# Performance work log

Hardware: AMD Instinct MI355X
Metric: run time of the kernel (lower is better)

The kernel has to match this reference:

```python
import jax, jax.numpy as jnp
import numpy as np

T = 16384       # tokens (flattened leading dims)
D_IN = 1024     # in_features
D_OUT = 1024    # out_features
E = 8           # n_models (experts)


def setup_inputs() -> dict:
    key = jax.random.key(0)
    kx, ki, kw, kb = jax.random.split(key, 4)
    x = jax.random.normal(kx, (T, D_IN), dtype=jnp.float32)
    idxs = jax.random.randint(ki, (T,), 0, E, dtype=jnp.int32)
    # Per-expert Linear params (nn.Linear default-ish init scale)
    scale = 1.0 / np.sqrt(D_IN)
    W = jax.random.uniform(kw, (E, D_IN, D_OUT), dtype=jnp.float32, minval=-scale, maxval=scale)
    b = jax.random.uniform(kb, (E, D_OUT), dtype=jnp.float32, minval=-scale, maxval=scale)
    return {"x": x, "idxs": idxs, "W": W, "b": b}


def reference(x, idxs, W, b):
    # Original: for each expert i, y[idxs==i] = Linear_i(x[idxs==i]); return relu(y).
    # Equivalent math: each token t gets expert idxs[t]'s linear.
    # Compute all experts densely (E is small), then gather the assigned row.
    ys = jnp.einsum('ti,eio->eto', x, W) + b[:, None, :]   # [E, T, D_OUT]
    y = ys[idxs, jnp.arange(x.shape[0])]                    # [T, D_OUT] pick assigned expert
    return jax.nn.relu(y)
```

## Files before the change

kernel.cpp:

```cpp
#include <hip/hip_runtime.h>
#include <hip/hip_bf16.h>
#include <stdint.h>


#define T_TOK 16384
#define DIN   1024
#define DOUT  1024
#define NE    8
#define BM    128
#define BN    128
#define BK    64
#define TPX   17
#define MAX_TILES 136
#define MP_MAX (T_TOK + NE * BM)

typedef __attribute__((ext_vector_type(8))) short short8;
typedef __attribute__((ext_vector_type(4))) short short4v;
typedef __attribute__((ext_vector_type(4))) float floatx4;
typedef __attribute__((ext_vector_type(4))) int int4v;

__device__ __forceinline__ short f2b(float f) {
  return __builtin_bit_cast(short, __float2bfloat16(f));
}
__device__ __forceinline__ float b2f(unsigned short u) {
  unsigned v = ((unsigned)u) << 16;
  return __builtin_bit_cast(float, v);
}
__device__ __forceinline__ void glds16(const void* g, void* l) {
  __builtin_amdgcn_global_load_lds(
      (__attribute__((address_space(1))) void*)g,
      (__attribute__((address_space(3))) void*)l, 16, 0, 0);
}

#define FLAG_OFF    0
#define NTILES_OFF  64
#define TABLE_OFF   1024
#define TPAD_OFF    8192
#define WT_OFF      81920
#define XB_OFF      16859136
#define WS_NEED     (16859136UL + (size_t)T_TOK * DIN * 2)

#define TRANS_BLOCKS 512
#define CONV_BLOCKS  1024

__global__ __launch_bounds__(1024) void k_front(
    const unsigned short* __restrict__ xu, const int* __restrict__ idxs,
    const void* __restrict__ Wsrc, short* __restrict__ Wt, short* __restrict__ xb,
    int* __restrict__ flag, int* __restrict__ ntiles,
    int4v* __restrict__ table, int* __restrict__ tpad) {
  __shared__ int fS;
  __shared__ unsigned short tile[128][130];
  __shared__ int wtot[16][NE], waveBase[16][NE];
  __shared__ int totS[NE], padS[NE + 1];

  int tid = threadIdx.x;
  if (tid == 0) fS = 0;
  __syncthreads();
  if (tid < 256) {
    int ex = (xu[tid] >> 7) & 0xFF;
    if (ex >= 0xC0) atomicOr(&fS, 1);
  }
  __syncthreads();
  int fp32 = fS;

  if (blockIdx.x >= 1 + TRANS_BLOCKS) {
    if (!fp32) return;
    int b2 = blockIdx.x - (1 + TRANS_BLOCKS);
    size_t base = ((size_t)b2 * 1024 + tid) * 16;
    const float* src = (const float*)xu + base;
    floatx4 a0 = *(const floatx4*)(src + 0);
    floatx4 a1 = *(const floatx4*)(src + 4);
    floatx4 a2 = *(const floatx4*)(src + 8);
    floatx4 a3 = *(const floatx4*)(src + 12);
    short8 o0, o1;
    #pragma unroll
    for (int j = 0; j < 4; ++j) {
      o0[j] = f2b(a0[j]); o0[4 + j] = f2b(a1[j]);
      o1[j] = f2b(a2[j]); o1[4 + j] = f2b(a3[j]);
    }
    *(short8*)(xb + base) = o0;
    *(short8*)(xb + base + 8) = o1;
    return;
  }

  if (blockIdx.x != 0) {
    int b = blockIdx.x - 1;
    int e = b >> 6, kt = (b >> 3) & 7, nt8 = b & 7;
    size_t ibase = (size_t)e * DIN * DOUT + (size_t)(kt * 128) * DOUT + nt8 * 128;
    int k = tid >> 3, n16 = (tid & 7) * 16;
    if (fp32) {
      const float* p = (const float*)Wsrc + ibase + (size_t)k * DOUT + n16;
      #pragma unroll
      for (int g = 0; g < 4; ++g) {
        floatx4 a = *(const floatx4*)(p + g * 4);
        #pragma unroll
        for (int j = 0; j < 4; ++j) tile[k][n16 + g * 4 + j] = (unsigned short)f2b(a[j]);
      }
    } else {
      const short* p = (const short*)Wsrc + ibase + (size_t)k * DOUT + n16;
      #pragma unroll
      for (int g = 0; g < 2; ++g) {
        short8 v = *(const short8*)(p + g * 8);
        #pragma unroll
        for (int j = 0; j < 8; ++j) tile[k][n16 + g * 8 + j] = (unsigned short)v[j];
      }
    }
    __syncthreads();
    int n = tid >> 3, k16 = (tid & 7) * 16;
    short8 o0, o1;
    #pragma unroll
    for (int j = 0; j < 8; ++j) {
      o0[j] = (short)tile[k16 + j][n];
      o1[j] = (short)tile[k16 + 8 + j][n];
    }
    size_t obase = (size_t)e * DOUT * DIN + (size_t)(nt8 * 128 + n) * DIN + kt * 128 + k16;
    *(short8*)(Wt + obase) = o0;
    *(short8*)(Wt + obase + 8) = o1;
    return;
  }

  int lane = tid & 63, w = tid >> 6;
  if (tid == 0) *flag = fp32;

  int c[NE];
  #pragma unroll
  for (int e = 0; e < NE; ++e) c[e] = 0;
  const int4v* iv = (const int4v*)idxs;
  int4v vv[4];
  #pragma unroll
  for (int it = 0; it < 4; ++it) {
    vv[it] = iv[tid * 4 + it];
    ++c[vv[it].x]; ++c[vv[it].y]; ++c[vv[it].z]; ++c[vv[it].w];
  }
  int incl[NE];
  #pragma unroll
  for (int e = 0; e < NE; ++e) {
    incl[e] = c[e];
    #pragma unroll
    for (int d = 1; d < 64; d <<= 1) {
      int o = __shfl_up(incl[e], d);
      if (lane >= d) incl[e] += o;
    }
  }
  if (lane == 63) {
    #pragma unroll
    for (int e = 0; e < NE; ++e) wtot[w][e] = incl[e];
  }
  __syncthreads();
  if (tid < NE) {
    int s = 0;
    for (int ww = 0; ww < 16; ++ww) s += wtot[ww][tid];
    totS[tid] = s;
  }
  __syncthreads();
  if (tid == 0) {
    int p = 0, tc = 0;
    for (int e = 0; e < NE; ++e) {
      padS[e] = p;
      int cn = totS[e];
      int nmt = (cn + BM - 1) >> 7;
      for (int m = 0; m < nmt; ++m) table[tc++] = (int4v){e, p + m * BM, 0, 0};
      p += nmt * BM;
    }
    padS[NE] = p;
    *ntiles = tc;
  }
  __syncthreads();
  if (tid < 128) {
    int ww = tid >> 3, e = tid & 7;
    int s = padS[e];
    for (int wp = 0; wp < ww; ++wp) s += wtot[wp][e];
    waveBase[ww][e] = s;
  }
  __syncthreads();
  int base[NE];
  #pragma unroll
  for (int e = 0; e < NE; ++e) base[e] = waveBase[w][e] + incl[e] - c[e];
  #pragma unroll
  for (int it = 0; it < 4; ++it) {
    #pragma unroll
    for (int cm = 0; cm < 4; ++cm) {
      int te = vv[it][cm];
      int tk = tid * 16 + it * 4 + cm;
      #pragma unroll
      for (int e0 = 0; e0 < NE; ++e0)
        if (te == e0) tpad[base[e0]++] = tk;
    }
  }
  #pragma unroll
  for (int e = 0; e < NE; ++e) {
    int start = padS[e] + totS[e];
    int len = padS[e + 1] - start;
    if (tid < len) tpad[start + tid] = -1;
  }
}

__launch_bounds__(256, 4)
__global__ void k_gemm(const void* __restrict__ xv, const short* __restrict__ xb,
                       const void* __restrict__ bv,
                       const short* __restrict__ Wt, const int* __restrict__ tpad,
                       const int* __restrict__ ntilesp, const int4v* __restrict__ table,
                       const int* __restrict__ flagp, void* __restrict__ outv) {
  int bid = blockIdx.x;
  int xcd = bid & 7;
  int s = bid >> 3;
  int nt = s & 7;
  int ti = s >> 3;
  int t = xcd * TPX + ti;
  if (t >= *ntilesp) return;
  int4v te = table[t];
  int e = te.x, arow0 = te.y;
  int fp32 = *flagp;

  int tid = threadIdx.x;
  int lane = tid & 63;
  int wave = tid >> 6;

  __shared__ short lA[BM * BK];
  __shared__ short lB[BN * BK];
  __shared__ int tokS[BM];

  if (tid < BM) tokS[tid] = tpad[arow0 + tid];
  __syncthreads();

  const short* WtE = Wt + (size_t)e * DOUT * DIN + (size_t)(nt * BN) * DIN;
  const char* aBase = fp32 ? (const char*)xb : (const char*)xv;

  const char* aG[4];
  const short* bG[4];
  char *aL[4], *bL[4];
  #pragma unroll
  for (int s4 = 0; s4 < 4; ++s4) {
    int fl = tid + s4 * 256;
    int r = fl >> 3, p = fl & 7;
    int kc = p ^ (r & 7);
    int tok = tokS[r];
    if (tok < 0) tok = 0;
    aG[s4] = aBase + (size_t)tok * (DIN * 2) + kc * 16;
    aL[s4] = (char*)lA + (s4 * 256 + wave * 64) * 16;
    bG[s4] = WtE + (size_t)r * DIN + kc * 8;
    bL[s4] = (char*)lB + (s4 * 256 + wave * 64) * 16;
  }

  int wm = wave & 1, wn = wave >> 1;
  int lrow = lane & 15, q = lane >> 4;
  int aOff[4][2], bOff[4][2];
  #pragma unroll
  for (int i = 0; i < 4; ++i) {
    int m = wm * 64 + i * 16 + lrow;
    #pragma unroll
    for (int h = 0; h < 2; ++h)
      aOff[i][h] = m * BK + (((h * 4 + q) ^ (m & 7)) * 8);
  }
  #pragma unroll
  for (int j = 0; j < 4; ++j) {
    int n = wn * 64 + j * 16 + lrow;
    #pragma unroll
    for (int h = 0; h < 2; ++h)
      bOff[j][h] = n * BK + (((h * 4 + q) ^ (n & 7)) * 8);
  }

  floatx4 acc[4][4];
  #pragma unroll
  for (int i = 0; i < 4; ++i)
    #pragma unroll
    for (int j = 0; j < 4; ++j)
      acc[i][j] = (floatx4){0.f, 0.f, 0.f, 0.f};

  for (int k0 = 0; k0 < DIN; k0 += BK) {
    __syncthreads();
    #pragma unroll
    for (int s4 = 0; s4 < 4; ++s4) glds16(bG[s4] + k0, bL[s4]);
    #pragma unroll
    for (int s4 = 0; s4 < 4; ++s4) glds16(aG[s4] + k0 * 2, aL[s4]);
    __syncthreads();
    #pragma unroll
    for (int h = 0; h < 2; ++h) {
      short8 af[4], bf[4];
      #pragma unroll
      for (int i = 0; i < 4; ++i) af[i] = *(const short8*)(lA + aOff[i][h]);
      #pragma unroll
      for (int j = 0; j < 4; ++j) bf[j] = *(const short8*)(lB + bOff[j][h]);
      #pragma unroll
      for (int i = 0; i < 4; ++i)
        #pragma unroll
        for (int j = 0; j < 4; ++j)
          acc[i][j] = __builtin_amdgcn_mfma_f32_16x16x32_bf16(bf[j], af[i], acc[i][j], 0, 0, 0);
    }
  }

  #pragma unroll
  for (int i = 0; i < 4; ++i) {
    int tok = tokS[wm * 64 + i * 16 + lrow];
    if (tok < 0) continue;
    size_t rowb = (size_t)tok * DOUT + nt * BN + wn * 64 + q * 4;
    #pragma unroll
    for (int j = 0; j < 4; ++j) {
      int n = nt * BN + wn * 64 + j * 16 + q * 4;
      if (fp32) {
        floatx4 b4 = *(const floatx4*)((const float*)bv + e * DOUT + n);
        floatx4 o;
        #pragma unroll
        for (int r = 0; r < 4; ++r) {
          float v = acc[i][j][r] + b4[r];
          o[r] = v > 0.f ? v : 0.f;
        }
        *(floatx4*)((float*)outv + rowb + j * 16) = o;
      } else {
        short4v b4 = *(const short4v*)((const short*)bv + e * DOUT + n);
        short4v o;
        #pragma unroll
        for (int r = 0; r < 4; ++r) {
          float v = acc[i][j][r] + b2f((unsigned short)b4[r]);
          o[r] = f2b(v > 0.f ? v : 0.f);
        }
        *(short4v*)((short*)outv + rowb + j * 16) = o;
      }
    }
  }
}

__global__ void k_fallback(const void* __restrict__ xv, const int* __restrict__ idxs,
                           const void* __restrict__ Wv, const void* __restrict__ bv,
                           void* __restrict__ outv) {
  __shared__ float xrow[DIN];
  __shared__ int sflag;
  int t = blockIdx.x;
  int e = idxs[t];
  if (threadIdx.x == 0) {
    const unsigned short* u = (const unsigned short*)xv;
    int f = 0;
    for (int i = 0; i < 256; ++i) { int ex = (u[i] >> 7) & 0xFF; if (ex >= 0xC0) f = 1; }
    sflag = f;
  }
  __syncthreads();
  int fp32 = sflag;
  for (int i = threadIdx.x; i < DIN; i += 256)
    xrow[i] = fp32 ? ((const float*)xv)[(size_t)t * DIN + i]
                   : b2f(((const unsigned short*)xv)[(size_t)t * DIN + i]);
  __syncthreads();
  float a[4] = {0.f, 0.f, 0.f, 0.f};
  for (int k = 0; k < DIN; ++k) {
    float xk = xrow[k];
    size_t wb = (size_t)e * DIN * DOUT + (size_t)k * DOUT + threadIdx.x;
    #pragma unroll
    for (int j = 0; j < 4; ++j) {
      float w = fp32 ? ((const float*)Wv)[wb + j * 256]
                     : b2f(((const unsigned short*)Wv)[wb + j * 256]);
      a[j] += xk * w;
    }
  }
  #pragma unroll
  for (int j = 0; j < 4; ++j) {
    int n = threadIdx.x + j * 256;
    float bias = fp32 ? ((const float*)bv)[e * DOUT + n]
                      : b2f(((const unsigned short*)bv)[e * DOUT + n]);
    float v = a[j] + bias;
    v = v > 0.f ? v : 0.f;
    size_t o = (size_t)t * DOUT + n;
    if (fp32) ((float*)outv)[o] = v;
    else      ((short*)outv)[o] = f2b(v);
  }
}

extern "C" void kernel_launch(void* const* d_in, const int* in_sizes, int n_in,
                              void* d_out, int out_size, void* d_ws, size_t ws_size,
                              hipStream_t stream) {
  const void* x    = d_in[0];
  const int*  idxs = (const int*)d_in[1];
  const void* W    = d_in[2];
  const void* bias = d_in[3];

  if (ws_size < WS_NEED) {
    k_fallback<<<T_TOK, 256, 0, stream>>>(x, idxs, W, bias, d_out);
    return;
  }
  char* ws = (char*)d_ws;
  int* flag    = (int*)(ws + FLAG_OFF);
  int* ntiles  = (int*)(ws + NTILES_OFF);
  int4v* table = (int4v*)(ws + TABLE_OFF);
  int* tpad    = (int*)(ws + TPAD_OFF);
  short* Wt    = (short*)(ws + WT_OFF);
  short* xb    = (short*)(ws + XB_OFF);

  k_front<<<1 + TRANS_BLOCKS + CONV_BLOCKS, 1024, 0, stream>>>(
      (const unsigned short*)x, idxs, W, Wt, xb, flag, ntiles, table, tpad);
  k_gemm<<<8 * 8 * TPX, 256, 0, stream>>>(x, xb, bias, Wt, tpad, ntiles, table, flag, d_out);
}
```

Measured before the change: 202.0 us.

## Double-buffer LDS tiles to overlap global-to-LDS loads with MFMA compute

```diff
diff --git a/kernel.cpp b/kernel.cpp
--- a/kernel.cpp
+++ b/kernel.cpp
@@ -195,7 +195,17 @@
   }
 }
 
-__launch_bounds__(256, 4)
+#define STAGE(bb, k0)                                                       \
+  {                                                                         \
+    _Pragma("unroll")                                                       \
+    for (int s4 = 0; s4 < 4; ++s4)                                          \
+      glds16(bG[s4] + (k0), (char*)lB[bb] + ldsOff[s4]);                    \
+    _Pragma("unroll")                                                       \
+    for (int s4 = 0; s4 < 4; ++s4)                                          \
+      glds16(aG[s4] + (size_t)(k0) * 2, (char*)lA[bb] + ldsOff[s4]);        \
+  }
+
+__launch_bounds__(256, 2)
 __global__ void k_gemm(const void* __restrict__ xv, const short* __restrict__ xb,
                        const void* __restrict__ bv,
                        const short* __restrict__ Wt, const int* __restrict__ tpad,
@@ -216,8 +226,8 @@
   int lane = tid & 63;
   int wave = tid >> 6;
 
-  __shared__ short lA[BM * BK];
-  __shared__ short lB[BN * BK];
+  __shared__ short lA[2][BM * BK];
+  __shared__ short lB[2][BN * BK];
   __shared__ int tokS[BM];
 
   if (tid < BM) tokS[tid] = tpad[arow0 + tid];
@@ -228,7 +238,7 @@
 
   const char* aG[4];
   const short* bG[4];
-  char *aL[4], *bL[4];
+  int ldsOff[4];
   #pragma unroll
   for (int s4 = 0; s4 < 4; ++s4) {
     int fl = tid + s4 * 256;
@@ -237,9 +247,8 @@
     int tok = tokS[r];
     if (tok < 0) tok = 0;
     aG[s4] = aBase + (size_t)tok * (DIN * 2) + kc * 16;
-    aL[s4] = (char*)lA + (s4 * 256 + wave * 64) * 16;
     bG[s4] = WtE + (size_t)r * DIN + kc * 8;
-    bL[s4] = (char*)lB + (s4 * 256 + wave * 64) * 16;
+    ldsOff[s4] = (s4 * 256 + wave * 64) * 16;
   }
 
   int wm = wave & 1, wn = wave >> 1;
@@ -267,26 +276,27 @@
     for (int j = 0; j < 4; ++j)
       acc[i][j] = (floatx4){0.f, 0.f, 0.f, 0.f};
 
-  for (int k0 = 0; k0 < DIN; k0 += BK) {
-    __syncthreads();
-    #pragma unroll
-    for (int s4 = 0; s4 < 4; ++s4) glds16(bG[s4] + k0, bL[s4]);
-    #pragma unroll
-    for (int s4 = 0; s4 < 4; ++s4) glds16(aG[s4] + k0 * 2, aL[s4]);
-    __syncthreads();
+  STAGE(0, 0);
+  asm volatile("s_waitcnt vmcnt(0)\n\ts_barrier" ::: "memory");
+
+  int cur = 0;
+  for (int kt = 0; kt < DIN / BK; ++kt) {
+    if (kt < DIN / BK - 1) STAGE(cur ^ 1, (kt + 1) * BK);
     #pragma unroll
     for (int h = 0; h < 2; ++h) {
       short8 af[4], bf[4];
       #pragma unroll
-      for (int i = 0; i < 4; ++i) af[i] = *(const short8*)(lA + aOff[i][h]);
-      #pragma unroll
-      for (int j = 0; j < 4; ++j) bf[j] = *(const short8*)(lB + bOff[j][h]);
+      for (int i = 0; i < 4; ++i) af[i] = *(const short8*)(&lA[cur][0] + aOff[i][h]);
+      #pragma unroll
+      for (int j = 0; j < 4; ++j) bf[j] = *(const short8*)(&lB[cur][0] + bOff[j][h]);
       #pragma unroll
       for (int i = 0; i < 4; ++i)
         #pragma unroll
         for (int j = 0; j < 4; ++j)
           acc[i][j] = __builtin_amdgcn_mfma_f32_16x16x32_bf16(bf[j], af[i], acc[i][j], 0, 0, 0);
     }
+    asm volatile("s_waitcnt vmcnt(0)\n\ts_barrier" ::: "memory");
+    cur ^= 1;
   }
 
   #pragma unroll
```

Measured after the change: 222.8 us. 10.3% more time.
